# Optimization experiments

Measured on AMD Instinct MI355X. Metric: run time of the kernel, lower is better.

## Reference

```python
import jax, jax.numpy as jnp
import numpy as np

EPS = 1e-10
V_NODES = 50000
E_EDGES = 25000
NNZ = 600000
S = 8   # num_subspace
K = 16  # dim_subspace
NUM_STEP = 4
TAU = 1.0


def setup_inputs() -> dict:
    key = jax.random.key(0)
    k1, k2, k3, k4 = jax.random.split(key, 4)
    node_embedding = 0.1 * jax.random.normal(k1, (V_NODES, S * K), dtype=jnp.float32)
    gumbel = jax.random.gumbel(k2, (V_NODES, S, K), dtype=jnp.float32)
    V_idx = jax.random.randint(k3, (NNZ,), 0, V_NODES, dtype=jnp.int32)
    E_idx = jax.random.randint(k4, (NNZ,), 0, E_EDGES, dtype=jnp.int32)
    return {"node_embedding": node_embedding, "gumbel": gumbel,
            "V_idx": V_idx, "E_idx": E_idx}


def scatter_mean(src, index, num_segments):
    # src: (nnz, D); segment mean with empty segments -> 0 (torch_scatter semantics)
    s = jax.ops.segment_sum(src, index, num_segments=num_segments)
    cnt = jax.ops.segment_sum(jnp.ones((src.shape[0], 1), src.dtype), index,
                              num_segments=num_segments)
    return s / jnp.maximum(cnt, 1.0)


def discrimination(X):
    # X: (N, S, K); cosine similarity over the data axis between subspace columns
    norms = jnp.sqrt(jnp.sum(X * X, axis=0))          # (S, K)
    G = jnp.einsum('nsi,nsj->sij', X, X)              # (S, K, K)
    denom = jnp.maximum(norms[:, :, None] * norms[:, None, :], EPS)
    C = G / denom
    P = jax.nn.softmax(C, axis=2)
    diag = jnp.diagonal(P, axis1=1, axis2=2)          # (S, K)
    return jnp.mean(-jnp.log(diag))


def reference(node_embedding, gumbel, V_idx, E_idx):
    logits = node_embedding.reshape(V_NODES, S, K)
    X0 = jax.nn.softmax((logits + gumbel) / TAU, axis=2)   # gumbel-softmax (soft)
    Xj = X0.reshape(V_NODES, S * K)
    loss_local = jnp.float32(0.0)
    loss_global = jnp.float32(0.0)
    for _ in range(NUM_STEP):
        Yj = scatter_mean(Xj[V_idx], E_idx, E_EDGES)        # (E, S*K)
        _Yj = Yj.reshape(E_EDGES, S, K)
        loss_local += jnp.mean(-jnp.sum(_Yj * jnp.log(_Yj + EPS), axis=2))
        p_Y = jnp.sum(_Yj, axis=0) / E_EDGES                # (S, K)
        loss_global += -jnp.mean(-jnp.sum(p_Y * jnp.log(p_Y + EPS), axis=1)) \
                       + discrimination(_Yj)
        Xg = scatter_mean(Yj[E_idx], V_idx, V_NODES)        # (V, S*K)
        _Xj = Xg.reshape(V_NODES, S, K)
        loss_local += jnp.mean(-jnp.sum(_Xj * jnp.log(_Xj + EPS), axis=2))
        p_X = jnp.sum(_Xj, axis=0) / V_NODES
        loss_global += -jnp.mean(-jnp.sum(p_X * jnp.log(p_X + EPS), axis=1)) \
                       + discrimination(_Xj)
        Xj = Xg
    return loss_local, loss_global
```

## Files before the change

kernel.cpp:

```cpp
#include <hip/hip_runtime.h>
#include <hip/hip_bf16.h>
#include <hip/hip_fp16.h>
#include <math.h>

#define V_NODES 50000
#define E_EDGES 25000
#define NNZ     600000
#define S_SUB   8
#define K_SUB   16
#define DD      128
#define NUM_STEP 4
#define EPSF    1e-10f

#define STATS_STRIDE 2177
#define NBLK 256

#define NTILE_E 25
#define NTILE_V 49
#define NTILES  (NTILE_E + NTILE_V)

#define FILL_BPG 256

typedef unsigned short pack_t;

__device__ inline __half2 u2h(pack_t u) {
    unsigned int bits = ((unsigned)(u & 0x7f) << 7) | ((unsigned)(u & 0x7f00) << 15);
    return __builtin_bit_cast(__half2, bits);
}
__device__ inline pack_t pack2(float a, float b) {
    unsigned short ha = __half_as_ushort(__float2half_rn(a * 0.00390625f));
    unsigned short hb = __half_as_ushort(__float2half_rn(b * 0.00390625f));
    unsigned short ra = (unsigned short)((ha + 0x3F + ((ha >> 7) & 1)) >> 7);
    unsigned short rb = (unsigned short)((hb + 0x3F + ((hb >> 7) & 1)) >> 7);
    return (pack_t)(ra | (rb << 8));
}

__global__ void softmax16_kernel(const float* __restrict__ emb,
                                 const float* __restrict__ gum,
                                 pack_t* __restrict__ X) {
    int i2 = blockIdx.x * blockDim.x + threadIdx.x;
    if (i2 >= V_NODES * 64) return;
    const float2* e2 = (const float2*)emb;
    const float2* g2 = (const float2*)gum;
    float2 e = e2[i2], g = g2[i2];
    float xa = e.x + g.x, xb = e.y + g.y;
    float m = fmaxf(xa, xb);
    #pragma unroll
    for (int off = 1; off < 8; off <<= 1) m = fmaxf(m, __shfl_xor(m, off, 8));
    float ea = expf(xa - m), eb = expf(xb - m);
    float s = ea + eb;
    #pragma unroll
    for (int off = 1; off < 8; off <<= 1) s += __shfl_xor(s, off, 8);
    float inv = 1.0f / s;
    X[i2] = pack2(ea * inv, eb * inv);
}

__global__ void hist_kernel(const int* __restrict__ Vi, const int* __restrict__ Ei,
                            int* __restrict__ cntV, int* __restrict__ cntE,
                            int* __restrict__ rankV, int* __restrict__ rankE) {
    int n = blockIdx.x * blockDim.x + threadIdx.x;
    if (n >= NNZ) return;
    rankV[n] = atomicAdd(&cntV[Vi[n]], 1);
    rankE[n] = atomicAdd(&cntE[Ei[n]], 1);
}

__global__ void scanA_kernel(const int* __restrict__ cntE, const int* __restrict__ cntV,
                             int* __restrict__ offE, int* __restrict__ offV,
                             int* __restrict__ sums) {
    int b = blockIdx.x;
    bool isE = b < NTILE_E;
    const int* cnt = isE ? cntE : cntV;
    int* off       = isE ? offE : offV;
    int N          = isE ? E_EDGES : V_NODES;
    int tile       = isE ? b : b - NTILE_E;

    int t = threadIdx.x, lane = t & 63, w = t >> 6;
    int i = tile * 1024 + t;
    int v = (i < N) ? ((cnt[i] + 7) & ~7) : 0;
    int x = v;
    #pragma unroll
    for (int d = 1; d < 64; d <<= 1) {
        int u = __shfl_up(x, d, 64);
        if (lane >= d) x += u;
    }
    __shared__ int wsum[16];
    if (lane == 63) wsum[w] = x;
    __syncthreads();
    if (t == 0) {
        int acc = 0;
        #pragma unroll
        for (int k = 0; k < 16; ++k) { int tk = wsum[k]; wsum[k] = acc; acc += tk; }
    }
    __syncthreads();
    int excl = wsum[w] + x - v;
    if (i < N) off[i] = excl;
    if (t == 1023) sums[b] = excl + v;
}

__global__ void scanB_kernel(int* __restrict__ sums) {
    if (threadIdx.x == 0) {
        int acc = 0;
        for (int k = 0; k < NTILE_E; ++k) { int t = sums[k]; sums[k] = acc; acc += t; }
        acc = 0;
        for (int k = NTILE_E; k < NTILES; ++k) { int t = sums[k]; sums[k] = acc; acc += t; }
    }
}

__global__ void scanC_kernel(int* __restrict__ offE, int* __restrict__ offV,
                             const int* __restrict__ sums) {
    int b = blockIdx.x;
    bool isE = b < NTILE_E;
    int* off = isE ? offE : offV;
    int N    = isE ? E_EDGES : V_NODES;
    int tile = isE ? b : b - NTILE_E;
    int i = tile * 1024 + threadIdx.x;
    if (i < N) off[i] += sums[b];
}

__global__ void fill_kernel(const int* __restrict__ Vi, const int* __restrict__ Ei,
                            const int* __restrict__ offE, const int* __restrict__ offV,
                            const int* __restrict__ rankE, const int* __restrict__ rankV,
                            unsigned short* __restrict__ listE,
                            unsigned short* __restrict__ listV) {
    int g  = blockIdx.x & 7;
    int bg = blockIdx.x >> 3;
    int eLo = g * (E_EDGES / 8), eHi = eLo + (E_EDGES / 8);
    int vLo = g * (V_NODES / 8), vHi = vLo + (V_NODES / 8);
    for (int n = bg * 256 + threadIdx.x; n < NNZ; n += FILL_BPG * 256) {
        int e = __builtin_nontemporal_load(&Ei[n]);
        int v = __builtin_nontemporal_load(&Vi[n]);
        if (e >= eLo && e < eHi) {
            int r = __builtin_nontemporal_load(&rankE[n]);
            listE[offE[e] + r] = (unsigned short)v;
        }
        if (v >= vLo && v < vHi) {
            int r = __builtin_nontemporal_load(&rankV[n]);
            listV[offV[v] + r] = (unsigned short)e;
        }
    }
}

__global__ __launch_bounds__(1024) void gather_stats(
        const pack_t* __restrict__ src, pack_t* __restrict__ dst,
        const unsigned short* __restrict__ list, const int* __restrict__ off,
        const int* __restrict__ cnt, int N, float* __restrict__ partials) {
    int t = threadIdx.x;
    int w = t >> 6;
    int lane = t & 63;
    int gw = blockIdx.x * 16 + w;
    const int NW = NBLK * 16;

    float ent = 0.f;
    float colx = 0.f, coly = 0.f;
    float g0[16], g1[16];
    #pragma unroll
    for (int j = 0; j < 16; ++j) { g0[j] = 0.f; g1[j] = 0.f; }

    for (int row0 = gw; row0 < N; row0 += NW) {
        int row = __builtin_amdgcn_readfirstlane(row0);
        int o   = __builtin_amdgcn_readfirstlane(off[row]);
        int deg = __builtin_amdgcn_readfirstlane(cnt[row]);

        float ax = 0.f, ay = 0.f;
        for (int k = 0; k < deg; k += 8) {
            uint4 wv = *(const uint4*)(list + o + k);
            unsigned wa0 = wv.x, wa1 = wv.y, wa2 = wv.z, wa3 = wv.w;
            __half2 h = __builtin_bit_cast(__half2, 0u);
            if (k + 8 <= deg) {
                #pragma unroll
                for (int j = 0; j < 8; ++j) {
                    unsigned wj = (j < 2) ? wa0 : (j < 4) ? wa1 : (j < 6) ? wa2 : wa3;
                    int idx = (int)((wj >> ((j & 1) * 16)) & 0xffffu);
                    h = __hadd2(h, u2h(src[(size_t)idx * 64 + lane]));
                }
            } else {
                int rem = deg - k;
                #pragma unroll
                for (int j = 0; j < 8; ++j) {
                    unsigned wj = (j < 2) ? wa0 : (j < 4) ? wa1 : (j < 6) ? wa2 : wa3;
                    int idx = (int)((wj >> ((j & 1) * 16)) & 0xffffu);
                    __half2 v = u2h(src[(size_t)idx * 64 + lane]);
                    h = (j < rem) ? __hadd2(h, v) : h;
                }
            }
            float2 f = __half22float2(h);
            ax += f.x; ay += f.y;
        }
        float inv = 256.0f / fmaxf((float)deg, 1.0f);
        float yx = ax * inv;
        float yy = ay * inv;
        dst[(size_t)row * 64 + lane] = pack2(yx, yy);

        ent -= yx * __logf(yx + EPSF) + yy * __logf(yy + EPSF);
        colx += yx; coly += yy;
        #pragma unroll
        for (int jj = 0; jj < 8; ++jj) {
            float zx = __shfl(yx, jj, 8);
            float zy = __shfl(yy, jj, 8);
            g0[2*jj]   += yx * zx;  g0[2*jj+1] += yx * zy;
            g1[2*jj]   += yy * zx;  g1[2*jj+1] += yy * zy;
        }
    }

    float* part = partials + (size_t)blockIdx.x * STATS_STRIDE;
    __shared__ float red[1024];

    red[t] = ent; __syncthreads();
    for (int st = 512; st > 0; st >>= 1) {
        if (t < st) red[t] += red[t + st];
        __syncthreads();
    }
    if (t == 0) part[0] = red[0];
    __syncthreads();

    red[t] = colx; __syncthreads();
    if (t < 64) {
        float v = 0.f;
        #pragma unroll
        for (int k2 = 0; k2 < 16; ++k2) v += red[k2*64 + t];
        part[1 + 2*t] = v;
    }
    __syncthreads();
    red[t] = coly; __syncthreads();
    if (t < 64) {
        float v = 0.f;
        #pragma unroll
        for (int k2 = 0; k2 < 16; ++k2) v += red[k2*64 + t];
        part[1 + 2*t + 1] = v;
    }
    __syncthreads();

    for (int j = 0; j < 16; ++j) {
        red[t] = g0[j]; __syncthreads();
        if (t < 64) {
            float v = 0.f;
            #pragma unroll
            for (int k2 = 0; k2 < 16; ++k2) v += red[k2*64 + t];
            part[129 + (t>>3)*256 + (2*(t&7))*16 + j] = v;
        }
        __syncthreads();
        red[t] = g1[j]; __syncthreads();
        if (t < 64) {
            float v = 0.f;
            #pragma unroll
            for (int k2 = 0; k2 < 16; ++k2) v += red[k2*64 + t];
            part[129 + (t>>3)*256 + (2*(t&7)+1)*16 + j] = v;
        }
        __syncthreads();
    }
}

__global__ void reduce_all_kernel(const float* __restrict__ partials,
                                  float* __restrict__ stats) {
    int u = blockIdx.x * blockDim.x + threadIdx.x;
    if (u >= 8 * STATS_STRIDE) return;
    int side = u / STATS_STRIDE, e = u - side * STATS_STRIDE;
    const float* p = partials + (size_t)side * NBLK * STATS_STRIDE + e;
    float acc = 0.f;
    for (int b = 0; b < NBLK; ++b)
        acc += p[(size_t)b * STATS_STRIDE];
    stats[side * STATS_STRIDE + e] = acc;
}

__global__ void loss_kernel(const float* __restrict__ stats, float* __restrict__ out) {
    int t = threadIdx.x;
    float acc_l = 0.f, acc_g = 0.f;

    if (t < 8) {
        float N = (t & 1) ? (float)V_NODES : (float)E_EDGES;
        acc_l = stats[t * STATS_STRIDE] / (N * (float)S_SUB);
    }

    for (int u = t; u < 8 * 128; u += blockDim.x) {
        int side = u >> 7, d = u & 127;
        float N = (side & 1) ? (float)V_NODES : (float)E_EDGES;
        float p = stats[side * STATS_STRIDE + 1 + d] / N;
        acc_g += p * logf(p + EPSF) / (float)S_SUB;
    }

    for (int u = t; u < 8 * 8 * 16; u += blockDim.x) {
        int side = u >> 7;
        int s = (u >> 4) & 7;
        int i = u & 15;
        const float* G = stats + side * STATS_STRIDE + 129 + s * 256;
        float nii = sqrtf(G[i * 16 + i]);
        float C[16];
        float m = -INFINITY;
        #pragma unroll
        for (int j = 0; j < 16; ++j) {
            float njj = sqrtf(G[j * 16 + j]);
            float c = G[i * 16 + j] / fmaxf(nii * njj, EPSF);
            C[j] = c;
            m = fmaxf(m, c);
        }
        float sum = 0.f;
        #pragma unroll
        for (int j = 0; j < 16; ++j) sum += expf(C[j] - m);
        float lse = logf(sum) + m;
        acc_g += (lse - C[i]) / (float)(S_SUB * K_SUB);
    }

    __shared__ float redl[256], redg[256];
    redl[t] = acc_l; redg[t] = acc_g; __syncthreads();
    for (int st = 128; st > 0; st >>= 1) {
        if (t < st) { redl[t] += redl[t + st]; redg[t] += redg[t + st]; }
        __syncthreads();
    }
    if (t == 0) { out[0] = redl[0]; out[1] = redg[0]; }
}

extern "C" void kernel_launch(void* const* d_in, const int* in_sizes, int n_in,
                              void* d_out, int out_size, void* d_ws, size_t ws_size,
                              hipStream_t stream) {
    const float* emb = (const float*)d_in[0];
    const float* gum = (const float*)d_in[1];
    const int*   Vi  = (const int*)d_in[2];
    const int*   Ei  = (const int*)d_in[3];
    float* out = (float*)d_out;

    char* ws = (char*)d_ws;
    size_t off = 0;
    pack_t* X = (pack_t*)(ws + off);    off += (size_t)V_NODES * 64 * sizeof(pack_t);
    pack_t* Y = (pack_t*)(ws + off);    off += (size_t)E_EDGES * 64 * sizeof(pack_t);
    unsigned short* listE = (unsigned short*)(ws + off);
    off += ((size_t)NNZ + 8 * E_EDGES) * 2;
    unsigned short* listV = (unsigned short*)(ws + off);
    off += ((size_t)NNZ + 8 * V_NODES) * 2;
    int* cntE  = (int*)(ws + off);      off += (size_t)E_EDGES * 4;
    int* cntV  = (int*)(ws + off);      off += (size_t)V_NODES * 4;
    int* offE  = (int*)(ws + off);      off += (size_t)E_EDGES * 4;
    int* offV  = (int*)(ws + off);      off += (size_t)V_NODES * 4;
    int* rankE = (int*)(ws + off);      off += (size_t)NNZ * 4;
    int* rankV = (int*)(ws + off);      off += (size_t)NNZ * 4;
    int* sums  = (int*)(ws + off);      off += (size_t)NTILES * 4;
    float* stats = (float*)(ws + off);  off += (size_t)8 * STATS_STRIDE * 4;
    float* partials = (float*)(ws + off);
    off += (size_t)8 * NBLK * STATS_STRIDE * 4;

    hipMemsetAsync(cntE, 0, ((size_t)E_EDGES + V_NODES) * 4, stream);

    softmax16_kernel<<<(V_NODES * 64 + 255) / 256, 256, 0, stream>>>(emb, gum, X);
    hist_kernel<<<(NNZ + 255) / 256, 256, 0, stream>>>(Vi, Ei, cntV, cntE, rankV, rankE);
    scanA_kernel<<<NTILES, 1024, 0, stream>>>(cntE, cntV, offE, offV, sums);
    scanB_kernel<<<1, 64, 0, stream>>>(sums);
    scanC_kernel<<<NTILES, 1024, 0, stream>>>(offE, offV, sums);
    fill_kernel<<<8 * FILL_BPG, 256, 0, stream>>>(Vi, Ei, offE, offV, rankE, rankV,
                                                  listE, listV);

    const size_t PSIDE = (size_t)NBLK * STATS_STRIDE;
    for (int step = 0; step < NUM_STEP; ++step) {
        gather_stats<<<NBLK, 1024, 0, stream>>>(X, Y, listE, offE, cntE, E_EDGES,
                                                partials + (2*step) * PSIDE);
        gather_stats<<<NBLK, 1024, 0, stream>>>(Y, X, listV, offV, cntV, V_NODES,
                                                partials + (2*step + 1) * PSIDE);
    }

    reduce_all_kernel<<<(8 * STATS_STRIDE + 255) / 256, 256, 0, stream>>>(partials, stats);
    loss_kernel<<<1, 256, 0, stream>>>(stats, out);
}
```

Before: 387.2 us.

## Vectorize softmax, shrink rank arrays, fold scan into scanC, prefetch gather rows

The softmax kernel now handles four elements per thread with float4 loads and 32-bit packed stores. The rank arrays shrink to 16-bit, and fill drops its nontemporal loads. The single-thread scanB launch is removed, and each scanC block now sums the preceding tile totals itself. gather_stats software-prefetches the next row's offset, degree and first index vector so list loads overlap the current row's gather, at the cost of extra registers and a redundant prefetch past the end.

```diff
diff --git a/kernel.cpp b/kernel.cpp
--- a/kernel.cpp
+++ b/kernel.cpp
@@ -35,33 +35,34 @@
     return (pack_t)(ra | (rb << 8));
 }
 
-__global__ void softmax16_kernel(const float* __restrict__ emb,
-                                 const float* __restrict__ gum,
-                                 pack_t* __restrict__ X) {
-    int i2 = blockIdx.x * blockDim.x + threadIdx.x;
-    if (i2 >= V_NODES * 64) return;
-    const float2* e2 = (const float2*)emb;
-    const float2* g2 = (const float2*)gum;
-    float2 e = e2[i2], g = g2[i2];
-    float xa = e.x + g.x, xb = e.y + g.y;
-    float m = fmaxf(xa, xb);
+__global__ void softmax16_kernel(const float4* __restrict__ emb4,
+                                 const float4* __restrict__ gum4,
+                                 unsigned int* __restrict__ X4) {
+    int i = blockIdx.x * blockDim.x + threadIdx.x;
+    if (i >= V_NODES * 32) return;
+    float4 e = emb4[i], g = gum4[i];
+    float a = e.x + g.x, b = e.y + g.y, c = e.z + g.z, d = e.w + g.w;
+    float m = fmaxf(fmaxf(a, b), fmaxf(c, d));
     #pragma unroll
-    for (int off = 1; off < 8; off <<= 1) m = fmaxf(m, __shfl_xor(m, off, 8));
-    float ea = expf(xa - m), eb = expf(xb - m);
-    float s = ea + eb;
+    for (int off = 1; off < 4; off <<= 1) m = fmaxf(m, __shfl_xor(m, off, 4));
+    float ea = expf(a - m), eb = expf(b - m), ec = expf(c - m), ed = expf(d - m);
+    float s = (ea + eb) + (ec + ed);
     #pragma unroll
-    for (int off = 1; off < 8; off <<= 1) s += __shfl_xor(s, off, 8);
+    for (int off = 1; off < 4; off <<= 1) s += __shfl_xor(s, off, 4);
     float inv = 1.0f / s;
-    X[i2] = pack2(ea * inv, eb * inv);
+    unsigned int lo = pack2(ea * inv, eb * inv);
+    unsigned int hi = pack2(ec * inv, ed * inv);
+    X4[i] = lo | (hi << 16);
 }
 
 __global__ void hist_kernel(const int* __restrict__ Vi, const int* __restrict__ Ei,
                             int* __restrict__ cntV, int* __restrict__ cntE,
-                            int* __restrict__ rankV, int* __restrict__ rankE) {
+                            unsigned short* __restrict__ rankV,
+                            unsigned short* __restrict__ rankE) {
     int n = blockIdx.x * blockDim.x + threadIdx.x;
     if (n >= NNZ) return;
-    rankV[n] = atomicAdd(&cntV[Vi[n]], 1);
-    rankE[n] = atomicAdd(&cntE[Ei[n]], 1);
+    rankV[n] = (unsigned short)atomicAdd(&cntV[Vi[n]], 1);
+    rankE[n] = (unsigned short)atomicAdd(&cntE[Ei[n]], 1);
 }
 
 __global__ void scanA_kernel(const int* __restrict__ cntE, const int* __restrict__ cntV,
@@ -97,15 +98,6 @@
     if (t == 1023) sums[b] = excl + v;
 }
 
-__global__ void scanB_kernel(int* __restrict__ sums) {
-    if (threadIdx.x == 0) {
-        int acc = 0;
-        for (int k = 0; k < NTILE_E; ++k) { int t = sums[k]; sums[k] = acc; acc += t; }
-        acc = 0;
-        for (int k = NTILE_E; k < NTILES; ++k) { int t = sums[k]; sums[k] = acc; acc += t; }
-    }
-}
-
 __global__ void scanC_kernel(int* __restrict__ offE, int* __restrict__ offV,
                              const int* __restrict__ sums) {
     int b = blockIdx.x;
@@ -113,13 +105,23 @@
     int* off = isE ? offE : offV;
     int N    = isE ? E_EDGES : V_NODES;
     int tile = isE ? b : b - NTILE_E;
+
+    __shared__ int base;
+    if (threadIdx.x == 0) {
+        int s0 = isE ? 0 : NTILE_E;
+        int acc = 0;
+        for (int j = s0; j < b; ++j) acc += sums[j];
+        base = acc;
+    }
+    __syncthreads();
     int i = tile * 1024 + threadIdx.x;
-    if (i < N) off[i] += sums[b];
+    if (i < N) off[i] += base;
 }
 
 __global__ void fill_kernel(const int* __restrict__ Vi, const int* __restrict__ Ei,
                             const int* __restrict__ offE, const int* __restrict__ offV,
-                            const int* __restrict__ rankE, const int* __restrict__ rankV,
+                            const unsigned short* __restrict__ rankE,
+                            const unsigned short* __restrict__ rankV,
                             unsigned short* __restrict__ listE,
                             unsigned short* __restrict__ listV) {
     int g  = blockIdx.x & 7;
@@ -127,16 +129,12 @@
     int eLo = g * (E_EDGES / 8), eHi = eLo + (E_EDGES / 8);
     int vLo = g * (V_NODES / 8), vHi = vLo + (V_NODES / 8);
     for (int n = bg * 256 + threadIdx.x; n < NNZ; n += FILL_BPG * 256) {
-        int e = __builtin_nontemporal_load(&Ei[n]);
-        int v = __builtin_nontemporal_load(&Vi[n]);
-        if (e >= eLo && e < eHi) {
-            int r = __builtin_nontemporal_load(&rankE[n]);
-            listE[offE[e] + r] = (unsigned short)v;
-        }
-        if (v >= vLo && v < vHi) {
-            int r = __builtin_nontemporal_load(&rankV[n]);
-            listV[offV[v] + r] = (unsigned short)e;
-        }
+        int e = Ei[n];
+        int v = Vi[n];
+        if (e >= eLo && e < eHi)
+            listE[offE[e] + (int)rankE[n]] = (unsigned short)v;
+        if (v >= vLo && v < vHi)
+            listV[offV[v] + (int)rankV[n]] = (unsigned short)e;
     }
 }
 
@@ -156,35 +154,75 @@
     #pragma unroll
     for (int j = 0; j < 16; ++j) { g0[j] = 0.f; g1[j] = 0.f; }
 
-    for (int row0 = gw; row0 < N; row0 += NW) {
-        int row = __builtin_amdgcn_readfirstlane(row0);
-        int o   = __builtin_amdgcn_readfirstlane(off[row]);
-        int deg = __builtin_amdgcn_readfirstlane(cnt[row]);
+    int o = 0, deg = 0;
+    uint4 q_cur{0,0,0,0};
+    if (gw < N) {
+        int r0 = __builtin_amdgcn_readfirstlane(gw);
+        o   = __builtin_amdgcn_readfirstlane(off[r0]);
+        deg = __builtin_amdgcn_readfirstlane(cnt[r0]);
+        q_cur = *(const uint4*)(list + o);
+    }
+
+    for (int base = gw; base < N; base += NW) {
+        int row = __builtin_amdgcn_readfirstlane(base);
+        int nbase = base + NW;
+        int o_n = 0, deg_n = 0;
+        if (nbase < N) {
+            int rn = __builtin_amdgcn_readfirstlane(nbase);
+            o_n   = __builtin_amdgcn_readfirstlane(off[rn]);
+            deg_n = __builtin_amdgcn_readfirstlane(cnt[rn]);
+        }
+        uint4 q_next = *(const uint4*)(list + o_n);
 
         float ax = 0.f, ay = 0.f;
-        for (int k = 0; k < deg; k += 8) {
-            uint4 wv = *(const uint4*)(list + o + k);
-            unsigned wa0 = wv.x, wa1 = wv.y, wa2 = wv.z, wa3 = wv.w;
-            __half2 h = __builtin_bit_cast(__half2, 0u);
-            if (k + 8 <= deg) {
-                #pragma unroll
-                for (int j = 0; j < 8; ++j) {
-                    unsigned wj = (j < 2) ? wa0 : (j < 4) ? wa1 : (j < 6) ? wa2 : wa3;
-                    int idx = (int)((wj >> ((j & 1) * 16)) & 0xffffu);
-                    h = __hadd2(h, u2h(src[(size_t)idx * 64 + lane]));
+        if (deg > 0) {
+            {
+                unsigned wa0 = q_cur.x, wa1 = q_cur.y, wa2 = q_cur.z, wa3 = q_cur.w;
+                __half2 h = __builtin_bit_cast(__half2, 0u);
+                if (deg >= 8) {
+                    #pragma unroll
+                    for (int j = 0; j < 8; ++j) {
+                        unsigned wj = (j < 2) ? wa0 : (j < 4) ? wa1 : (j < 6) ? wa2 : wa3;
+                        int idx = (int)((wj >> ((j & 1) * 16)) & 0xffffu);
+                        h = __hadd2(h, u2h(src[(size_t)idx * 64 + lane]));
+                    }
+                } else {
+                    int rem = deg;
+                    #pragma unroll
+                    for (int j = 0; j < 8; ++j) {
+                        unsigned wj = (j < 2) ? wa0 : (j < 4) ? wa1 : (j < 6) ? wa2 : wa3;
+                        int idx = (int)((wj >> ((j & 1) * 16)) & 0xffffu);
+                        __half2 v = u2h(src[(size_t)idx * 64 + lane]);
+                        h = (j < rem) ? __hadd2(h, v) : h;
+                    }
                 }
-            } else {
-                int rem = deg - k;
-                #pragma unroll
-                for (int j = 0; j < 8; ++j) {
-                    unsigned wj = (j < 2) ? wa0 : (j < 4) ? wa1 : (j < 6) ? wa2 : wa3;
-                    int idx = (int)((wj >> ((j & 1) * 16)) & 0xffffu);
-                    __half2 v = u2h(src[(size_t)idx * 64 + lane]);
-                    h = (j < rem) ? __hadd2(h, v) : h;
+                float2 f = __half22float2(h);
+                ax += f.x; ay += f.y;
+            }
+            for (int k = 8; k < deg; k += 8) {
+                uint4 wv = *(const uint4*)(list + o + k);
+                unsigned wa0 = wv.x, wa1 = wv.y, wa2 = wv.z, wa3 = wv.w;
+                __half2 h = __builtin_bit_cast(__half2, 0u);
+                if (k + 8 <= deg) {
+                    #pragma unroll
+                    for (int j = 0; j < 8; ++j) {
+                        unsigned wj = (j < 2) ? wa0 : (j < 4) ? wa1 : (j < 6) ? wa2 : wa3;
+                        int idx = (int)((wj >> ((j & 1) * 16)) & 0xffffu);
+                        h = __hadd2(h, u2h(src[(size_t)idx * 64 + lane]));
+                    }
+                } else {
+                    int rem = deg - k;
+                    #pragma unroll
+                    for (int j = 0; j < 8; ++j) {
+                        unsigned wj = (j < 2) ? wa0 : (j < 4) ? wa1 : (j < 6) ? wa2 : wa3;
+                        int idx = (int)((wj >> ((j & 1) * 16)) & 0xffffu);
+                        __half2 v = u2h(src[(size_t)idx * 64 + lane]);
+                        h = (j < rem) ? __hadd2(h, v) : h;
+                    }
                 }
+                float2 f = __half22float2(h);
+                ax += f.x; ay += f.y;
             }
-            float2 f = __half22float2(h);
-            ax += f.x; ay += f.y;
         }
         float inv = 256.0f / fmaxf((float)deg, 1.0f);
         float yx = ax * inv;
@@ -200,6 +238,8 @@
             g0[2*jj]   += yx * zx;  g0[2*jj+1] += yx * zy;
             g1[2*jj]   += yy * zx;  g1[2*jj+1] += yy * zy;
         }
+
+        o = o_n; deg = deg_n; q_cur = q_next;
     }
 
     float* part = partials + (size_t)blockIdx.x * STATS_STRIDE;
@@ -330,8 +370,8 @@
     int* cntV  = (int*)(ws + off);      off += (size_t)V_NODES * 4;
     int* offE  = (int*)(ws + off);      off += (size_t)E_EDGES * 4;
     int* offV  = (int*)(ws + off);      off += (size_t)V_NODES * 4;
-    int* rankE = (int*)(ws + off);      off += (size_t)NNZ * 4;
-    int* rankV = (int*)(ws + off);      off += (size_t)NNZ * 4;
+    unsigned short* rankE = (unsigned short*)(ws + off); off += (size_t)NNZ * 2;
+    unsigned short* rankV = (unsigned short*)(ws + off); off += (size_t)NNZ * 2;
     int* sums  = (int*)(ws + off);      off += (size_t)NTILES * 4;
     float* stats = (float*)(ws + off);  off += (size_t)8 * STATS_STRIDE * 4;
     float* partials = (float*)(ws + off);
@@ -339,10 +379,10 @@
 
     hipMemsetAsync(cntE, 0, ((size_t)E_EDGES + V_NODES) * 4, stream);
 
-    softmax16_kernel<<<(V_NODES * 64 + 255) / 256, 256, 0, stream>>>(emb, gum, X);
+    softmax16_kernel<<<(V_NODES * 32 + 255) / 256, 256, 0, stream>>>(
+        (const float4*)emb, (const float4*)gum, (unsigned int*)X);
     hist_kernel<<<(NNZ + 255) / 256, 256, 0, stream>>>(Vi, Ei, cntV, cntE, rankV, rankE);
     scanA_kernel<<<NTILES, 1024, 0, stream>>>(cntE, cntV, offE, offV, sums);
-    scanB_kernel<<<1, 64, 0, stream>>>(sums);
     scanC_kernel<<<NTILES, 1024, 0, stream>>>(offE, offV, sums);
     fill_kernel<<<8 * FILL_BPG, 256, 0, stream>>>(Vi, Ei, offE, offV, rankE, rankV,
                                                   listE, listV);
```

New measurement: 416.4 us. 1.08x slower.
